# Performance work log

Measured on AMD Instinct MI355X. Metric: run time of the kernel, lower is better.

## Reference

```python
import jax, jax.numpy as jnp
import numpy as np

B, H, W, C = 8, 64, 64, 256
C8 = C // 8  # query/key channels


def setup_inputs() -> dict:
    key = jax.random.key(0)
    ks = jax.random.split(key, 8)
    s = 0.02  # init scale for weights
    return {
        "x": jax.random.normal(ks[0], (B, H, W, C), dtype=jnp.float32),
        "Wq": jax.random.normal(ks[1], (C, C8), dtype=jnp.float32) * s,
        "bq": jnp.zeros((C8,), dtype=jnp.float32),
        "Wk": jax.random.normal(ks[2], (C, C8), dtype=jnp.float32) * s,
        "bk": jnp.zeros((C8,), dtype=jnp.float32),
        "Wv": jax.random.normal(ks[3], (C, C), dtype=jnp.float32) * s,
        "bv": jnp.zeros((C,), dtype=jnp.float32),
        "gamma": jnp.full((1,), 0.5, dtype=jnp.float32),
    }


def reference(x, Wq, bq, Wk, bk, Wv, bv, gamma):
    Bn, Hn, Wn, Cn = x.shape
    N = Hn * Wn
    xf = x.reshape(Bn, N, Cn)            # flatten spatial dims: [B, N, C]
    # 1x1 convs == per-pixel dense projections over channels
    q = xf @ Wq + bq                     # [B, N, C//8]
    k = xf @ Wk + bk                     # [B, N, C//8]
    v = xf @ Wv + bv                     # [B, N, C]
    # energy[b,i,j] = k_i . q_j  (matches tf.matmul(key, query, transpose_b=True))
    energy = jnp.einsum('bic,bjc->bij', k, q)   # [B, N, N]
    attn = jax.nn.softmax(energy, axis=-1)      # softmax over last axis
    # out_i = sum_j attn[i,j] * v_j  (intended SAGAN aggregation in NHWC layout)
    out = jnp.einsum('bij,bjc->bic', attn, v)   # [B, N, C]
    out = out.reshape(Bn, Hn, Wn, Cn)
    return gamma * out + x
```

## Files before the change

### kernel.cpp

```cpp
#include <hip/hip_runtime.h>

typedef __attribute__((ext_vector_type(8))) short short8;
typedef __attribute__((ext_vector_type(4))) float f32x4;
typedef __attribute__((ext_vector_type(16))) float f32x16;
typedef __attribute__((ext_vector_type(2))) unsigned int u32x2;
typedef __attribute__((ext_vector_type(4))) unsigned int u32x4;
typedef unsigned short u16;
typedef unsigned int u32;

#define MFMA16(a, b, c) __builtin_amdgcn_mfma_f32_16x16x32_bf16((a), (b), (c), 0, 0, 0)
#define MFMA32(a, b, c) __builtin_amdgcn_mfma_f32_32x32x16_bf16((a), (b), (c), 0, 0, 0)

#define BAR_VMEM() asm volatile("s_waitcnt vmcnt(0) lgkmcnt(0)\ns_barrier" ::: "memory")
#define BAR_LDS()  asm volatile("s_waitcnt lgkmcnt(0)\ns_barrier" ::: "memory")

#define BATCH 8
#define NTOK 4096
#define CDIM 256
#define CQK 32
#define LOG2E 1.4426950408889634f

__device__ __forceinline__ u16 f2bf(float f) {
  u32 u = __float_as_uint(f);
  return (u16)((u + 0x7FFFu + ((u >> 16) & 1u)) >> 16);
}
__device__ __forceinline__ u32 pack2(float a, float b) {
  const u32 ua = __float_as_uint(a) + 0x8000u;
  const u32 ub = __float_as_uint(b) + 0x8000u;
#if __has_builtin(__builtin_amdgcn_perm)
  return __builtin_amdgcn_perm(ub, ua, 0x07060302u);
#else
  return (ua >> 16) | (ub & 0xFFFF0000u);
#endif
}
__device__ __forceinline__ float fexp2(float x) {
#if __has_builtin(__builtin_amdgcn_exp2f)
  return __builtin_amdgcn_exp2f(x);
#else
  return exp2f(x);
#endif
}
__device__ __forceinline__ void gl_lds16(const u16* g, u16* l) {
  __builtin_amdgcn_global_load_lds(
      (const __attribute__((address_space(1))) unsigned int*)(g),
      (__attribute__((address_space(3))) unsigned int*)(l), 16, 0, 0);
}

__global__ void k_prep(const float* __restrict__ Wq, const float* __restrict__ bq,
                       const float* __restrict__ Wk, const float* __restrict__ bk,
                       const float* __restrict__ Wv, const float* __restrict__ bv,
                       u16* __restrict__ wtf, float* __restrict__ bias) {
  const int f = blockIdx.x;
  const int L = threadIdx.x;
  const int ct = f >> 3, ks = f & 7;
  const int o = ct * 16 + (L & 15);
  const int ch = ks * 32 + (L >> 4) * 8;
  short8 v8;
#pragma unroll
  for (int jj = 0; jj < 8; jj++) {
    const int c = ch + jj;
    float v;
    if (o < 32)       v = Wq[c * CQK + o];
    else if (o < 64)  v = Wk[c * CQK + (o - 32)];
    else              v = Wv[c * CDIM + (o - 64)];
    v8[jj] = (short)f2bf(v);
  }
  *(short8*)(wtf + (size_t)f * 512 + L * 8) = v8;
  if (f == 0) {
    for (int i = L; i < 320; i += 64) {
      if (i < 32)      bias[i] = bq[i];
      else if (i < 64) bias[i] = bk[i - 32];
      else             bias[i] = bv[i - 64];
    }
  }
}

__global__ __launch_bounds__(256, 2) void k_proj(
    const float* __restrict__ x, const u16* __restrict__ wtf,
    const float* __restrict__ bias,
    u16* __restrict__ q_ws, u16* __restrict__ k_ws, u16* __restrict__ vt_ws) {
  __shared__ u16 x_lds[64 * 264];
  __shared__ u16 vt_t[64 * 72];
  const int m0 = blockIdx.x * 64;
  const int tid = threadIdx.x;
  const int w = tid >> 6, L = tid & 63;
  const int lr = L & 15, q4 = L >> 4;

#pragma unroll
  for (int ii = 0; ii < 8; ii++) {
    const int e = (tid + 256 * ii) * 8;
    const int row = e >> 8, col = e & 255;
    const float* src = x + (size_t)(m0 + row) * CDIM + col;
    f32x4 a = *(const f32x4*)src;
    f32x4 b4 = *(const f32x4*)(src + 4);
    u32x4 pk;
    pk[0] = pack2(a[0], a[1]);
    pk[1] = pack2(a[2], a[3]);
    pk[2] = pack2(b4[0], b4[1]);
    pk[3] = pack2(b4[2], b4[3]);
    *(u32x4*)&x_lds[row * 264 + col] = pk;
  }
  __syncthreads();

  const int mrow = w * 16;
  f32x4 acc[20];
#pragma unroll
  for (int ct = 0; ct < 20; ct++) acc[ct] = (f32x4){0.f, 0.f, 0.f, 0.f};

#pragma unroll
  for (int ks = 0; ks < 8; ks++) {
    short8 a = *(const short8*)&x_lds[(mrow + lr) * 264 + ks * 32 + q4 * 8];
#pragma unroll
    for (int ct = 0; ct < 20; ct++) {
      short8 bf = *(const short8*)(wtf + ((size_t)(ct * 8 + ks)) * 512 + L * 8);
      acc[ct] = MFMA16(a, bf, acc[ct]);
    }
  }

#pragma unroll
  for (int ct = 0; ct < 4; ct++) {
    const float bb = bias[ct * 16 + lr];
    const int o = ct * 16 + lr;
#pragma unroll
    for (int r = 0; r < 4; r++) {
      const int row = m0 + mrow + q4 * 4 + r;
      float v = acc[ct][r] + bb;
      if (o < 32) q_ws[(size_t)row * CQK + o] = f2bf(v);
      else        k_ws[(size_t)row * CQK + (o - 32)] = f2bf(v * LOG2E);
    }
  }
  const int b = m0 >> 12, nloc = m0 & 4095;
  const int rb2 = ((lr >> 3) & 1) << 2;
#pragma unroll
  for (int cg = 0; cg < 4; cg++) {
    __syncthreads();
#pragma unroll
    for (int t4 = 0; t4 < 4; t4++) {
      const int ct = 4 + cg * 4 + t4;
      const float bb = bias[ct * 16 + lr];
      const int c_l = t4 * 16 + lr;
      const int n_base = (mrow + q4 * 4) ^ rb2;
      u32x2 pk;
      pk[0] = pack2(acc[ct][0] + bb, acc[ct][1] + bb);
      pk[1] = pack2(acc[ct][2] + bb, acc[ct][3] + bb);
      *(u32x2*)&vt_t[c_l * 72 + n_base] = pk;
    }
    __syncthreads();
#pragma unroll
    for (int i = 0; i < 2; i++) {
      const int gch = tid + 256 * i;
      const int c_l = gch >> 3, jc = gch & 7;
      short8 v = *(const short8*)&vt_t[c_l * 72 + jc * 8];
      *(short8*)(vt_ws + ((size_t)(b * CDIM + cg * 64 + c_l)) * NTOK + nloc + jc * 8) = v;
    }
  }
}

__global__ __launch_bounds__(256, 4) void k_attn(
    const float* __restrict__ x, const u16* __restrict__ q_ws,
    const u16* __restrict__ k_ws, const u16* __restrict__ vt_ws,
    const float* __restrict__ gamma, float* __restrict__ out) {
  __shared__ u16 vt_lds[2][128 * 64];
  __shared__ u16 p_lds[64 * 64];

  const int bid = blockIdx.x;
  const int b = bid & 7;
  const int chalf = (bid >> 3) & 1;
  const int it = bid >> 4;
  const int i0 = it * 64;
  const int c0 = chalf * 128;
  const int tid = threadIdx.x;
  const int w = tid >> 6, L = tid & 63;
  const int lr = L & 15, q4 = L >> 4;
  const int L31 = L & 31, Lhi = L >> 5, L7 = L & 7;
  const int ih = w & 1, cpair = w >> 1;

  const short8 a_k = *(const short8*)(k_ws +
      ((size_t)(b * NTOK + i0 + w * 16 + lr)) * CQK + q4 * 8);

  const int cl_base = tid >> 3;
  const int jc_sw = (tid & 7) ^ (cl_base & 7);
  const u16* vt_g = vt_ws + ((size_t)(b * CDIM + c0 + cl_base)) * NTOK + jc_sw * 8;
  const u16* q_base = q_ws + (size_t)b * NTOK * CQK;

  f32x16 o_acc[2];
#pragma unroll
  for (int t = 0; t < 2; t++)
#pragma unroll
    for (int e = 0; e < 16; e++) o_acc[t][e] = 0.f;
  float lsum = 0.f;

  u16* pw0 = p_lds + (w * 16 + lr) * 64 + (((q4 & 1) ^ ((lr >> 3) & 1)) << 2);
  const int q4h = q4 >> 1;

  short8 bqA[4], bqB[4];
#pragma unroll
  for (int t = 0; t < 4; t++)
    bqA[t] = *(const short8*)(q_base + (size_t)(t * 16 + lr) * CQK + q4 * 8);
#pragma unroll
  for (int ii = 0; ii < 4; ii++)
    gl_lds16(vt_g + (size_t)(ii * 32) * NTOK, &vt_lds[0][ii * 2048 + w * 512]);

#define ATTN_ITER(JT, VB_CUR, VB_NXT, BQ, BQN)                                   \
  do {                                                                           \
    const int j0 = (JT) * 64;                                                    \
    BAR_LDS();                         \
       \
    _Pragma("unroll")                                                            \
    for (int t = 0; t < 4; t++)                                                  \
      BQN[t] = *(const short8*)(q_base +                                         \
               (size_t)(j0 + 64 + t * 16 + lr) * CQK + q4 * 8);                  \
                  \
    f32x4 s[4];                                                                  \
    _Pragma("unroll")                                                            \
    for (int t = 0; t < 4; t++)                                                  \
      s[t] = MFMA16(BQ[t], a_k, ((f32x4){0.f, 0.f, 0.f, 0.f}));                  \
                   \
    _Pragma("unroll")                                                            \
    for (int t = 0; t < 4; t++) {                                                \
      const float p0 = fexp2(s[t][0]);                                           \
      const float p1 = fexp2(s[t][1]);                                           \
      const float p2 = fexp2(s[t][2]);                                           \
      const float p3 = fexp2(s[t][3]);                                           \
      lsum += (p0 + p1) + (p2 + p3);                                             \
      u32x2 pk;                                                                  \
      pk[0] = pack2(p0, p1);                                                     \
      pk[1] = pack2(p2, p3);                                                     \
      *(u32x2*)(pw0 + (((2 * t + q4h) ^ (lr & 7)) * 8)) = pk;                    \
    }                                                                            \
    BAR_VMEM();          \
              \
    if ((JT) < 63) {                                                             \
      _Pragma("unroll")                                                          \
      for (int ii = 0; ii < 4; ii++)                                             \
        gl_lds16(vt_g + (size_t)(ii * 32) * NTOK + (j0 + 64),                    \
                 &VB_NXT[ii * 2048 + w * 512]);                                  \
    }                                                                            \
            \
    _Pragma("unroll")                                                            \
    for (int ks = 0; ks < 4; ks++) {                                             \
      const int slot = (((ks * 2 + Lhi) ^ L7)) * 8;                              \
      short8 a_p = *(const short8*)(p_lds + (ih * 32 + L31) * 64 + slot);        \
      _Pragma("unroll")                                                          \
      for (int ct2 = 0; ct2 < 2; ct2++) {                                        \
        const int cl = (cpair * 2 + ct2) * 32 + L31;                             \
        short8 b_v = *(const short8*)(&VB_CUR[0] + cl * 64 + slot);              \
        o_acc[ct2] = MFMA32(a_p, b_v, o_acc[ct2]);                               \
      }                                                                          \
    }                                                                            \
  } while (0)

  for (int jt2 = 0; jt2 < 64; jt2 += 2) {
    ATTN_ITER(jt2,     vt_lds[0], vt_lds[1], bqA, bqB);
    ATTN_ITER(jt2 + 1, vt_lds[1], vt_lds[0], bqB, bqA);
  }
#undef ATTN_ITER

  float s2 = lsum;
  s2 += __shfl_xor(s2, 16);
  s2 += __shfl_xor(s2, 32);
  const float rl = 1.0f / s2;
  BAR_LDS();
  float* lp = (float*)p_lds;
  if (q4 == 0) lp[w * 16 + lr] = rl;
  BAR_LDS();

  float linv[16];
#pragma unroll
  for (int rg = 0; rg < 16; rg++)
    linv[rg] = lp[ih * 32 + (rg & 3) + 8 * (rg >> 2) + 4 * Lhi];

  const float g = gamma[0];
#pragma unroll
  for (int ct2 = 0; ct2 < 2; ct2++) {
    const int c = c0 + (cpair * 2 + ct2) * 32 + L31;
#pragma unroll
    for (int rg = 0; rg < 16; rg++) {
      const int i = i0 + ih * 32 + (rg & 3) + 8 * (rg >> 2) + 4 * Lhi;
      const size_t idx = ((size_t)(b * NTOK + i)) * CDIM + c;
      out[idx] = g * (o_acc[ct2][rg] * linv[rg]) + x[idx];
    }
  }
}

extern "C" void kernel_launch(void* const* d_in, const int* in_sizes, int n_in,
                              void* d_out, int out_size, void* d_ws, size_t ws_size,
                              hipStream_t stream) {
  const float* x  = (const float*)d_in[0];
  const float* Wq = (const float*)d_in[1];
  const float* bq = (const float*)d_in[2];
  const float* Wk = (const float*)d_in[3];
  const float* bk = (const float*)d_in[4];
  const float* Wv = (const float*)d_in[5];
  const float* bv = (const float*)d_in[6];
  const float* gamma = (const float*)d_in[7];
  float* out = (float*)d_out;

  char* ws = (char*)d_ws;
  u16* q_ws  = (u16*)(ws);
  u16* k_ws  = (u16*)(ws + (2u << 20));
  u16* vt_ws = (u16*)(ws + (4u << 20));
  u16* wtf   = (u16*)(ws + (20u << 20));
  float* bias = (float*)(ws + (20u << 20) + (256u << 10));

  k_prep<<<160, 64, 0, stream>>>(Wq, bq, Wk, bk, Wv, bv, wtf, bias);
  k_proj<<<512, 256, 0, stream>>>(x, wtf, bias, q_ws, k_ws, vt_ws);
  k_attn<<<1024, 256, 0, stream>>>(x, q_ws, k_ws, vt_ws, gamma, out);
}
```

Before: 230.7 us.

## Rewrite attention kernel to keep P in registers and drop LDS staging

The attention kernel is restructured so each wave owns 64 output channels for all 64 query rows. It computes the full score tile itself with 32x32 MFMAs and feeds the exp'd probabilities straight from registers into the PV MFMA as the B operand, reading V directly from global memory. This removes the LDS round trip for P and V, the per-iteration barriers, and the duplicated QK/exp work across the two channel halves, halving the grid. In exchange each wave recomputes scores for the whole tile, register pressure rises (launch bounds lowered to 2), and V loads go to global memory/cache without LDS sharing. The projection kernel's V transpose layout is changed to match the new fragment order.

```diff
diff --git a/kernel.cpp b/kernel.cpp
--- a/kernel.cpp
+++ b/kernel.cpp
@@ -10,9 +10,6 @@
 
 #define MFMA16(a, b, c) __builtin_amdgcn_mfma_f32_16x16x32_bf16((a), (b), (c), 0, 0, 0)
 #define MFMA32(a, b, c) __builtin_amdgcn_mfma_f32_32x32x16_bf16((a), (b), (c), 0, 0, 0)
-
-#define BAR_VMEM() asm volatile("s_waitcnt vmcnt(0) lgkmcnt(0)\ns_barrier" ::: "memory")
-#define BAR_LDS()  asm volatile("s_waitcnt lgkmcnt(0)\ns_barrier" ::: "memory")
 
 #define BATCH 8
 #define NTOK 4096
@@ -39,11 +36,6 @@
 #else
   return exp2f(x);
 #endif
-}
-__device__ __forceinline__ void gl_lds16(const u16* g, u16* l) {
-  __builtin_amdgcn_global_load_lds(
-      (const __attribute__((address_space(1))) unsigned int*)(g),
-      (__attribute__((address_space(3))) unsigned int*)(l), 16, 0, 0);
 }
 
 __global__ void k_prep(const float* __restrict__ Wq, const float* __restrict__ bq,
@@ -130,7 +122,6 @@
     }
   }
   const int b = m0 >> 12, nloc = m0 & 4095;
-  const int rb2 = ((lr >> 3) & 1) << 2;
 #pragma unroll
   for (int cg = 0; cg < 4; cg++) {
     __syncthreads();
@@ -139,7 +130,7 @@
       const int ct = 4 + cg * 4 + t4;
       const float bb = bias[ct * 16 + lr];
       const int c_l = t4 * 16 + lr;
-      const int n_base = (mrow + q4 * 4) ^ rb2;
+      const int n_base = mrow + (((q4 & 1) << 1) | (q4 >> 1)) * 4;
       u32x2 pk;
       pk[0] = pack2(acc[ct][0] + bb, acc[ct][1] + bb);
       pk[1] = pack2(acc[ct][2] + bb, acc[ct][3] + bb);
@@ -156,129 +147,138 @@
   }
 }
 
-__global__ __launch_bounds__(256, 4) void k_attn(
+__global__ __launch_bounds__(256, 2) void k_attn(
     const float* __restrict__ x, const u16* __restrict__ q_ws,
     const u16* __restrict__ k_ws, const u16* __restrict__ vt_ws,
     const float* __restrict__ gamma, float* __restrict__ out) {
-  __shared__ u16 vt_lds[2][128 * 64];
-  __shared__ u16 p_lds[64 * 64];
-
   const int bid = blockIdx.x;
   const int b = bid & 7;
-  const int chalf = (bid >> 3) & 1;
-  const int it = bid >> 4;
+  const int it = bid >> 3;
   const int i0 = it * 64;
-  const int c0 = chalf * 128;
   const int tid = threadIdx.x;
   const int w = tid >> 6, L = tid & 63;
-  const int lr = L & 15, q4 = L >> 4;
-  const int L31 = L & 31, Lhi = L >> 5, L7 = L & 7;
-  const int ih = w & 1, cpair = w >> 1;
-
-  const short8 a_k = *(const short8*)(k_ws +
-      ((size_t)(b * NTOK + i0 + w * 16 + lr)) * CQK + q4 * 8);
-
-  const int cl_base = tid >> 3;
-  const int jc_sw = (tid & 7) ^ (cl_base & 7);
-  const u16* vt_g = vt_ws + ((size_t)(b * CDIM + c0 + cl_base)) * NTOK + jc_sw * 8;
-  const u16* q_base = q_ws + (size_t)b * NTOK * CQK;
-
-  f32x16 o_acc[2];
-#pragma unroll
-  for (int t = 0; t < 2; t++)
-#pragma unroll
-    for (int e = 0; e < 16; e++) o_acc[t][e] = 0.f;
-  float lsum = 0.f;
-
-  u16* pw0 = p_lds + (w * 16 + lr) * 64 + (((q4 & 1) ^ ((lr >> 3) & 1)) << 2);
-  const int q4h = q4 >> 1;
-
-  short8 bqA[4], bqB[4];
-#pragma unroll
-  for (int t = 0; t < 4; t++)
-    bqA[t] = *(const short8*)(q_base + (size_t)(t * 16 + lr) * CQK + q4 * 8);
-#pragma unroll
-  for (int ii = 0; ii < 4; ii++)
-    gl_lds16(vt_g + (size_t)(ii * 32) * NTOK, &vt_lds[0][ii * 2048 + w * 512]);
-
-#define ATTN_ITER(JT, VB_CUR, VB_NXT, BQ, BQN)                                   \
-  do {                                                                           \
-    const int j0 = (JT) * 64;                                                    \
-    BAR_LDS();                         \
-       \
-    _Pragma("unroll")                                                            \
-    for (int t = 0; t < 4; t++)                                                  \
-      BQN[t] = *(const short8*)(q_base +                                         \
-               (size_t)(j0 + 64 + t * 16 + lr) * CQK + q4 * 8);                  \
-                  \
-    f32x4 s[4];                                                                  \
-    _Pragma("unroll")                                                            \
-    for (int t = 0; t < 4; t++)                                                  \
-      s[t] = MFMA16(BQ[t], a_k, ((f32x4){0.f, 0.f, 0.f, 0.f}));                  \
-                   \
-    _Pragma("unroll")                                                            \
-    for (int t = 0; t < 4; t++) {                                                \
-      const float p0 = fexp2(s[t][0]);                                           \
-      const float p1 = fexp2(s[t][1]);                                           \
-      const float p2 = fexp2(s[t][2]);                                           \
-      const float p3 = fexp2(s[t][3]);                                           \
-      lsum += (p0 + p1) + (p2 + p3);                                             \
-      u32x2 pk;                                                                  \
-      pk[0] = pack2(p0, p1);                                                     \
-      pk[1] = pack2(p2, p3);                                                     \
-      *(u32x2*)(pw0 + (((2 * t + q4h) ^ (lr & 7)) * 8)) = pk;                    \
-    }                                                                            \
-    BAR_VMEM();          \
-              \
-    if ((JT) < 63) {                                                             \
-      _Pragma("unroll")                                                          \
-      for (int ii = 0; ii < 4; ii++)                                             \
-        gl_lds16(vt_g + (size_t)(ii * 32) * NTOK + (j0 + 64),                    \
-                 &VB_NXT[ii * 2048 + w * 512]);                                  \
-    }                                                                            \
-            \
-    _Pragma("unroll")                                                            \
-    for (int ks = 0; ks < 4; ks++) {                                             \
-      const int slot = (((ks * 2 + Lhi) ^ L7)) * 8;                              \
-      short8 a_p = *(const short8*)(p_lds + (ih * 32 + L31) * 64 + slot);        \
-      _Pragma("unroll")                                                          \
-      for (int ct2 = 0; ct2 < 2; ct2++) {                                        \
-        const int cl = (cpair * 2 + ct2) * 32 + L31;                             \
-        short8 b_v = *(const short8*)(&VB_CUR[0] + cl * 64 + slot);              \
-        o_acc[ct2] = MFMA32(a_p, b_v, o_acc[ct2]);                               \
-      }                                                                          \
-    }                                                                            \
+  const int L31 = L & 31, Lhi = L >> 5;
+  const int c0 = w * 64;
+
+  const u16* qb = q_ws + (size_t)b * NTOK * CQK;
+  const u16* kb = k_ws + (size_t)b * NTOK * CQK;
+  const u16* vb = vt_ws + ((size_t)(b * CDIM + c0)) * NTOK;
+
+  short8 kf[2][2];
+#pragma unroll
+  for (int it2 = 0; it2 < 2; it2++)
+#pragma unroll
+    for (int ch2 = 0; ch2 < 2; ch2++)
+      kf[it2][ch2] = *(const short8*)(kb +
+          (size_t)(i0 + it2 * 32 + L31) * CQK + ch2 * 16 + Lhi * 8);
+
+  f32x16 acc[2][2];
+#pragma unroll
+  for (int a2 = 0; a2 < 2; a2++)
+#pragma unroll
+    for (int b2 = 0; b2 < 2; b2++)
+#pragma unroll
+      for (int e = 0; e < 16; e++) acc[a2][b2][e] = 0.f;
+  float lsum[2] = {0.f, 0.f};
+
+  short8 qf[2][2][2];
+#pragma unroll
+  for (int jt2 = 0; jt2 < 2; jt2++)
+#pragma unroll
+    for (int ch2 = 0; ch2 < 2; ch2++)
+      qf[0][jt2][ch2] = *(const short8*)(qb +
+          (size_t)(jt2 * 32 + L31) * CQK + ch2 * 16 + Lhi * 8);
+
+#define ATTN_ITER(JT, CUR)                                                      \
+  do {                                                                          \
+    const int j0 = (JT) * 64;                                                   \
+             \
+    short8 vf[2][4];                                                            \
+    _Pragma("unroll")                                                           \
+    for (int ct2 = 0; ct2 < 2; ct2++)                                           \
+      _Pragma("unroll")                                                         \
+      for (int kt = 0; kt < 4; kt++)                                            \
+        vf[ct2][kt] = *(const short8*)(vb +                                     \
+            (size_t)(ct2 * 32 + L31) * NTOK + j0 + kt * 16 + Lhi * 8);          \
+                \
+    {                                                                           \
+      const int jn = (j0 + 64) & (NTOK - 1);                                    \
+      _Pragma("unroll")                                                         \
+      for (int jt2 = 0; jt2 < 2; jt2++)                                         \
+        _Pragma("unroll")                                                       \
+        for (int ch2 = 0; ch2 < 2; ch2++)                                       \
+          qf[(CUR) ^ 1][jt2][ch2] = *(const short8*)(qb +                       \
+              (size_t)(jn + jt2 * 32 + L31) * CQK + ch2 * 16 + Lhi * 8);        \
+    }                                                                           \
+             \
+    short8 pf[2][4];                                                            \
+    _Pragma("unroll")                                                           \
+    for (int it2 = 0; it2 < 2; it2++) {                                         \
+      _Pragma("unroll")                                                         \
+      for (int jt2 = 0; jt2 < 2; jt2++) {                                       \
+        f32x16 st;                                                              \
+        _Pragma("unroll")                                                       \
+        for (int e = 0; e < 16; e++) st[e] = 0.f;                               \
+        st = MFMA32(qf[CUR][jt2][0], kf[it2][0], st);                           \
+        st = MFMA32(qf[CUR][jt2][1], kf[it2][1], st);                           \
+        float p[16];                                                            \
+        float ls = 0.f;                                                         \
+        _Pragma("unroll")                                                       \
+        for (int r = 0; r < 16; r++) {                                          \
+          p[r] = fexp2(st[r]);                                                  \
+          ls += p[r];                                                           \
+        }                                                                       \
+        lsum[it2] += ls;                                                        \
+        u32x4 lo, hi;                                                           \
+        _Pragma("unroll")                                                       \
+        for (int q2 = 0; q2 < 4; q2++) {                                        \
+          lo[q2] = pack2(p[2 * q2], p[2 * q2 + 1]);                             \
+          hi[q2] = pack2(p[8 + 2 * q2], p[9 + 2 * q2]);                         \
+        }                                                                       \
+        pf[it2][jt2 * 2 + 0] = __builtin_bit_cast(short8, lo);                  \
+        pf[it2][jt2 * 2 + 1] = __builtin_bit_cast(short8, hi);                  \
+      }                                                                         \
+    }                                                                           \
+                                                          \
+    _Pragma("unroll")                                                           \
+    for (int it2 = 0; it2 < 2; it2++)                                           \
+      _Pragma("unroll")                                                         \
+      for (int ct2 = 0; ct2 < 2; ct2++)                                         \
+        _Pragma("unroll")                                                       \
+        for (int kt = 0; kt < 4; kt++)                                          \
+          acc[it2][ct2] = MFMA32(vf[ct2][kt], pf[it2][kt], acc[it2][ct2]);      \
   } while (0)
 
-  for (int jt2 = 0; jt2 < 64; jt2 += 2) {
-    ATTN_ITER(jt2,     vt_lds[0], vt_lds[1], bqA, bqB);
-    ATTN_ITER(jt2 + 1, vt_lds[1], vt_lds[0], bqB, bqA);
+  for (int jt2x = 0; jt2x < 64; jt2x += 2) {
+    ATTN_ITER(jt2x, 0);
+    ATTN_ITER(jt2x + 1, 1);
   }
 #undef ATTN_ITER
 
-  float s2 = lsum;
-  s2 += __shfl_xor(s2, 16);
-  s2 += __shfl_xor(s2, 32);
-  const float rl = 1.0f / s2;
-  BAR_LDS();
-  float* lp = (float*)p_lds;
-  if (q4 == 0) lp[w * 16 + lr] = rl;
-  BAR_LDS();
-
-  float linv[16];
-#pragma unroll
-  for (int rg = 0; rg < 16; rg++)
-    linv[rg] = lp[ih * 32 + (rg & 3) + 8 * (rg >> 2) + 4 * Lhi];
-
   const float g = gamma[0];
-#pragma unroll
-  for (int ct2 = 0; ct2 < 2; ct2++) {
-    const int c = c0 + (cpair * 2 + ct2) * 32 + L31;
-#pragma unroll
-    for (int rg = 0; rg < 16; rg++) {
-      const int i = i0 + ih * 32 + (rg & 3) + 8 * (rg >> 2) + 4 * Lhi;
-      const size_t idx = ((size_t)(b * NTOK + i)) * CDIM + c;
-      out[idx] = g * (o_acc[ct2][rg] * linv[rg]) + x[idx];
+  float mul[2];
+#pragma unroll
+  for (int it2 = 0; it2 < 2; it2++) {
+    float s2 = lsum[it2] + __shfl_xor(lsum[it2], 32);
+    mul[it2] = g / s2;
+  }
+
+#pragma unroll
+  for (int it2 = 0; it2 < 2; it2++) {
+    const int row = i0 + it2 * 32 + L31;
+#pragma unroll
+    for (int ct2 = 0; ct2 < 2; ct2++) {
+#pragma unroll
+      for (int q2 = 0; q2 < 4; q2++) {
+        const int c = c0 + ct2 * 32 + 8 * q2 + 4 * Lhi;
+        const size_t idx = ((size_t)(b * NTOK + row)) * CDIM + c;
+        f32x4 x4 = *(const f32x4*)(x + idx);
+        f32x4 o4;
+#pragma unroll
+        for (int e = 0; e < 4; e++)
+          o4[e] = acc[it2][ct2][4 * q2 + e] * mul[it2] + x4[e];
+        *(f32x4*)(out + idx) = o4;
+      }
     }
   }
 }
@@ -305,5 +305,5 @@
 
   k_prep<<<160, 64, 0, stream>>>(Wq, bq, Wk, bk, Wv, bv, wtf, bias);
   k_proj<<<512, 256, 0, stream>>>(x, wtf, bias, q_ws, k_ws, vt_ws);
-  k_attn<<<1024, 256, 0, stream>>>(x, q_ws, k_ws, vt_ws, gamma, out);
-}
+  k_attn<<<512, 256, 0, stream>>>(x, q_ws, k_ws, vt_ws, gamma, out);
+}
```

Measured after the change: 277.4 us. 20.2% more time.
